# Optimization experiments

Hardware: AMD Instinct MI355X
Metric: run time of the kernel (lower is better)

The kernel has to match this reference:

```python
import jax, jax.numpy as jnp
import numpy as np

TOPK = 300
NUM_LEVELS = 3
GATE_TEMP = 1.0


def _normalized_grid(h, w):
    # matches torch: linspace(-1,1) meshgrid 'ij', stack (xx, yy) -> [h*w, 2]
    y = jnp.linspace(-1.0, 1.0, h, dtype=jnp.float32)
    x = jnp.linspace(-1.0, 1.0, w, dtype=jnp.float32)
    yy, xx = jnp.meshgrid(y, x, indexing='ij')
    return jnp.stack((xx, yy), axis=-1).reshape(h * w, 2)


def setup_inputs() -> dict:
    key = jax.random.key(0)
    ks = jax.random.split(key, 10)
    C, H_DIM, MAXL = 256, 256, 8
    shapes = [(8, C, 100, 152), (8, C, 50, 76), (8, C, 25, 38)]
    inp = {}
    for i, s in enumerate(shapes):
        inp[f'f{i}'] = jax.random.normal(ks[i], s, dtype=jnp.float32)
    inp['conv_w'] = jax.random.normal(ks[3], (C,), dtype=jnp.float32) * (1.0 / np.sqrt(C))
    inp['conv_b'] = jnp.zeros((1,), dtype=jnp.float32)
    inp['level_emb'] = jax.random.normal(ks[4], (MAXL, H_DIM), dtype=jnp.float32)
    qin = C + H_DIM + 3  # 515
    inp['w1'] = jax.random.normal(ks[5], (qin, H_DIM), dtype=jnp.float32) * (1.0 / np.sqrt(qin))
    inp['b1'] = jnp.zeros((H_DIM,), dtype=jnp.float32)
    inp['w2'] = jax.random.normal(ks[6], (H_DIM, H_DIM), dtype=jnp.float32) * (1.0 / np.sqrt(H_DIM))
    inp['b2'] = jnp.zeros((H_DIM,), dtype=jnp.float32)
    inp['gate_w'] = jax.random.normal(ks[7], (H_DIM, MAXL), dtype=jnp.float32) * (1.0 / np.sqrt(H_DIM))
    inp['gate_b'] = jnp.zeros((MAXL,), dtype=jnp.float32)
    inp['residual_scale'] = jnp.zeros((1,), dtype=jnp.float32)  # residual_scale_init=0.0
    return inp


def reference(f0, f1, f2, conv_w, conv_b, level_emb, w1, b1, w2, b2, gate_w, gate_b, residual_scale):
    levels = [f0, f1, f2]
    B = f0.shape[0]
    tok_s, tok_f, tok_p, tok_l = [], [], [], []
    for i, f in enumerate(levels):
        _, C, H, W = f.shape
        # 1x1 conv proxy objectness score -> [B, H*W]
        s = jnp.einsum('bchw,c->bhw', f, conv_w).reshape(B, H * W) + conv_b[0]
        tok_s.append(s)
        tok_f.append(f.reshape(B, C, H * W).transpose(0, 2, 1))       # [B, HW, C]
        tok_p.append(jnp.broadcast_to(_normalized_grid(H, W), (B, H * W, 2)))
        tok_l.append(jnp.full((B, H * W), i, dtype=jnp.int32))
    scores = jnp.concatenate(tok_s, axis=1)   # [B, N]
    feats = jnp.concatenate(tok_f, axis=1)    # [B, N, C]
    pos = jnp.concatenate(tok_p, axis=1)      # [B, N, 2]
    lvl = jnp.concatenate(tok_l, axis=1)      # [B, N]

    top_vals, top_idx = jax.lax.top_k(scores, TOPK)                     # [B, K]
    fk = jnp.take_along_axis(feats, top_idx[:, :, None], axis=1)        # [B, K, C]
    pk = jnp.take_along_axis(pos, top_idx[:, :, None], axis=1)          # [B, K, 2]
    lk = jnp.take_along_axis(lvl, top_idx, axis=1)                      # [B, K]
    sp = jax.nn.sigmoid(top_vals)                                       # [B, K]

    q = jnp.concatenate([fk, level_emb[lk], pk, sp[..., None]], axis=-1)  # [B, K, C+H+3]
    h = jax.nn.relu(q @ w1 + b1)
    h = jax.nn.relu(h @ w2 + b2)
    logits = (h @ gate_w + gate_b)[..., :NUM_LEVELS]                     # [B, K, L]
    gates = jax.nn.softmax(logits / GATE_TEMP, axis=-1)
    alpha = gates.mean(axis=1)                                           # [B, L]
    scale = 1.0 + residual_scale[0] * alpha                              # [B, L]

    outs = [f * scale[:, i][:, None, None, None] for i, f in enumerate(levels)]
    # flatten the output feature dict into one [B, sum(C*H*W)] array
    return jnp.concatenate([o.reshape(B, -1) for o in outs], axis=1)
```

## Files before the change

### kernel.cpp

```cpp
#include <hip/hip_runtime.h>
#include <hip/hip_bf16.h>

#define NTOK 19950
#define KTOP 300
#define NB 8
#define NQ (NB * KTOP)
#define QDIM 520
#define SCW 5225

typedef float f32x4 __attribute__((ext_vector_type(4)));

__device__ __forceinline__ uint32_t fkey(float f) {
    uint32_t u = __float_as_uint(f);
    return (u & 0x80000000u) ? ~u : (u | 0x80000000u);
}

__global__ __launch_bounds__(256) void score_kernel(
    const float* __restrict__ f0, const float* __restrict__ f1, const float* __restrict__ f2,
    const float* __restrict__ conv_w, const float* __restrict__ conv_b,
    float* __restrict__ scores)
{
    __shared__ float cw[256];
    cw[threadIdx.x] = conv_w[threadIdx.x];
    __syncthreads();
    int t = blockIdx.x * 256 + threadIdx.x;
    if (t >= NB * SCW) return;
    const int b = t / SCW;
    const int r = t - b * SCW;
    const float cb = conv_b[0];
    if (r < 3800) {
        const float* base = f0 + (size_t)b * 256 * 15200 + r * 4;
        float s0 = 0.f, s1 = 0.f, s2 = 0.f, s3 = 0.f;
        #pragma unroll 16
        for (int c = 0; c < 256; ++c) {
            float4 v = *reinterpret_cast<const float4*>(base + (size_t)c * 15200);
            float w = cw[c];
            s0 += v.x * w; s1 += v.y * w; s2 += v.z * w; s3 += v.w * w;
        }
        float* so = scores + b * NTOK + r * 4;
        so[0] = s0 + cb; so[1] = s1 + cb; so[2] = s2 + cb; so[3] = s3 + cb;
    } else if (r < 4750) {
        const int r1 = r - 3800;
        const float* base = f1 + (size_t)b * 256 * 3800 + r1 * 4;
        float s0 = 0.f, s1 = 0.f, s2 = 0.f, s3 = 0.f;
        #pragma unroll 16
        for (int c = 0; c < 256; ++c) {
            float4 v = *reinterpret_cast<const float4*>(base + (size_t)c * 3800);
            float w = cw[c];
            s0 += v.x * w; s1 += v.y * w; s2 += v.z * w; s3 += v.w * w;
        }
        float* so = scores + b * NTOK + 15200 + r1 * 4;
        so[0] = s0 + cb; so[1] = s1 + cb; so[2] = s2 + cb; so[3] = s3 + cb;
    } else {
        const int r2 = r - 4750;
        const float* base = f2 + (size_t)b * 256 * 950 + r2 * 2;
        float s0 = 0.f, s1 = 0.f;
        #pragma unroll 16
        for (int c = 0; c < 256; ++c) {
            float2 v = *reinterpret_cast<const float2*>(base + (size_t)c * 950);
            float w = cw[c];
            s0 += v.x * w; s1 += v.y * w;
        }
        float* so = scores + b * NTOK + 19000 + r2 * 2;
        so[0] = s0 + cb; so[1] = s1 + cb;
    }
}

__global__ __launch_bounds__(1024, 1) void topk_kernel(
    const float* __restrict__ scores, int* __restrict__ top_idx)
{
    __shared__ uint32_t key[NTOK];
    __shared__ int whist[16][256];
    __shared__ int suffix[257];
    __shared__ uint32_t s_prefix;
    __shared__ int s_Kr, s_cnt, s_tcnt;
    __shared__ int tie[1024];
    const int tid = threadIdx.x;
    const int wv = tid >> 6;
    const int b = blockIdx.x;
    const float* srow = scores + b * NTOK;
    for (int i = tid; i < NTOK; i += 1024) key[i] = fkey(srow[i]);
    if (tid == 0) { s_prefix = 0u; s_Kr = KTOP; suffix[256] = 0; }
    __syncthreads();
    uint32_t pmask = 0u;
    for (int pass = 0; pass < 4; ++pass) {
        const int shift = 24 - 8 * pass;
        for (int i = tid; i < 16 * 256; i += 1024) ((int*)whist)[i] = 0;
        __syncthreads();
        const uint32_t prefix = s_prefix;
        const int Kr = s_Kr;
        for (int i = tid; i < NTOK; i += 1024) {
            uint32_t k = key[i];
            if ((k & pmask) == prefix) atomicAdd(&whist[wv][(k >> shift) & 255], 1);
        }
        __syncthreads();
        if (tid < 256) {
            int s = 0;
            #pragma unroll
            for (int w = 0; w < 16; ++w) s += whist[w][tid];
            suffix[tid] = s;
        }
        __syncthreads();
        if (tid < 64) {
            const int c0 = suffix[tid * 4], c1 = suffix[tid * 4 + 1];
            const int c2 = suffix[tid * 4 + 2], c3 = suffix[tid * 4 + 3];
            const int tot = c0 + c1 + c2 + c3;
            int s = tot;
            #pragma unroll
            for (int off = 1; off < 64; off <<= 1) {
                int o = __shfl_down(s, off);
                if (tid + off < 64) s += o;
            }
            const int Sn = s - tot;
            suffix[tid * 4 + 3] = c3 + Sn;
            suffix[tid * 4 + 2] = c2 + c3 + Sn;
            suffix[tid * 4 + 1] = c1 + c2 + c3 + Sn;
            suffix[tid * 4 + 0] = tot + Sn;
        }
        __syncthreads();
        if (tid < 256) {
            int sgeq = suffix[tid];
            int sgt  = suffix[tid + 1];
            if (sgeq >= Kr && sgt < Kr) {
                s_prefix = prefix | ((uint32_t)tid << shift);
                s_Kr = Kr - sgt;
            }
        }
        __syncthreads();
        pmask |= (0xFFu << shift);
    }
    const uint32_t T = s_prefix;
    const int need = s_Kr;
    if (tid == 0) { s_cnt = 0; s_tcnt = 0; }
    __syncthreads();
    for (int i = tid; i < NTOK; i += 1024) {
        uint32_t k = key[i];
        if (k > T) {
            int p = atomicAdd(&s_cnt, 1);
            top_idx[b * KTOP + p] = i;
        } else if (k == T) {
            int p = atomicAdd(&s_tcnt, 1);
            if (p < 1024) tie[p] = i;
        }
    }
    __syncthreads();
    if (tid == 0) {
        int base = s_cnt;
        int tcnt = s_tcnt > 1024 ? 1024 : s_tcnt;
        for (int s = 0; s < need; ++s) {
            int mi = s;
            for (int u = s + 1; u < tcnt; ++u) if (tie[u] < tie[mi]) mi = u;
            int tmp = tie[s]; tie[s] = tie[mi]; tie[mi] = tmp;
            top_idx[b * KTOP + base + s] = tie[s];
        }
    }
}

#define QT 8
__global__ __launch_bounds__(512, 1) void mlp_kernel(
    const float* __restrict__ f0, const float* __restrict__ f1, const float* __restrict__ f2,
    const float* __restrict__ scores, const int* __restrict__ top_idx,
    const float* __restrict__ level_emb,
    const float* __restrict__ w1, const float* __restrict__ b1,
    const float* __restrict__ w2, const float* __restrict__ b2,
    const float* __restrict__ gate_w, const float* __restrict__ gate_b,
    float* __restrict__ G)
{
    __shared__ __align__(16) float q[QT][QDIM];
    __shared__ __align__(16) float part[QT][256];
    __shared__ __align__(16) float h[QT][256];
    __shared__ int s_b[QT], s_lvl[QT], s_hw[QT], s_HW[QT];
    const int tid = threadIdx.x;
    const int out = tid & 255;
    const int kh = tid >> 8;
    const int k0 = blockIdx.x * QT;

    if (tid < QT) {
        const int kk = k0 + tid;
        const int bq = kk / KTOP;
        const int idx = top_idx[kk];
        int lvl, hw, HWl, Wl, Hl;
        if (idx < 15200)      { lvl = 0; hw = idx;         HWl = 15200; Wl = 152; Hl = 100; }
        else if (idx < 19000) { lvl = 1; hw = idx - 15200; HWl = 3800;  Wl = 76;  Hl = 50;  }
        else                  { lvl = 2; hw = idx - 19000; HWl = 950;   Wl = 38;  Hl = 25;  }
        s_b[tid] = bq; s_lvl[tid] = lvl; s_hw[tid] = hw; s_HW[tid] = HWl;
        int hh = hw / Wl, ww = hw - hh * Wl;
        float x = -1.0f + 2.0f * (float)ww / (float)(Wl - 1);
        float y = -1.0f + 2.0f * (float)hh / (float)(Hl - 1);
        float sv = scores[bq * NTOK + idx];
        float sp = 1.0f / (1.0f + expf(-sv));
        q[tid][512] = x; q[tid][513] = y; q[tid][514] = sp;
        q[tid][515] = 0.0f; q[tid][516] = 0.0f; q[tid][517] = 0.0f;
        q[tid][518] = 0.0f; q[tid][519] = 0.0f;
    }
    __syncthreads();
    #pragma unroll
    for (int j = tid; j < QT * 256; j += 512) {
        const int t = j >> 8, c = j & 255;
        const int lvl = s_lvl[t];
        const float* f = (lvl == 0) ? f0 : ((lvl == 1) ? f1 : f2);
        q[t][c]       = f[((size_t)(s_b[t] * 256 + c)) * s_HW[t] + s_hw[t]];
        q[t][256 + c] = level_emb[lvl * 256 + c];
    }
    __syncthreads();

    float acc[QT];

    {
        #pragma unroll
        for (int t = 0; t < QT; ++t) acc[t] = 0.0f;
        const float* wp = w1 + (size_t)(kh * 256) * 256 + out;
        float a0 = wp[0], a1 = wp[256], a2 = wp[512], a3 = wp[768];
        for (int i4 = 0; i4 < 64; ++i4) {
            float c0 = a0, c1 = a1, c2 = a2, c3 = a3;
            const float* wn = wp + 1024;
            if (i4 < 63) { a0 = wn[0]; a1 = wn[256]; a2 = wn[512]; a3 = wn[768]; }
            wp = wn;
            const int kb = kh * 256 + i4 * 4;
            #pragma unroll
            for (int t = 0; t < QT; ++t) {
                float4 qv = *reinterpret_cast<const float4*>(&q[t][kb]);
                acc[t] += qv.x * c0 + qv.y * c1 + qv.z * c2 + qv.w * c3;
            }
        }
        if (kh) {
            for (int r = 512; r < 515; ++r) {
                float wv = w1[(size_t)r * 256 + out];
                #pragma unroll
                for (int t = 0; t < QT; ++t) acc[t] += q[t][r] * wv;
            }
            #pragma unroll
            for (int t = 0; t < QT; ++t) part[t][out] = acc[t];
        }
    }
    __syncthreads();
    if (kh == 0) {
        float bj = b1[out];
        #pragma unroll
        for (int t = 0; t < QT; ++t) h[t][out] = fmaxf(acc[t] + part[t][out] + bj, 0.0f);
    }
    __syncthreads();

    {
        #pragma unroll
        for (int t = 0; t < QT; ++t) acc[t] = 0.0f;
        const float* wp = w2 + (size_t)(kh * 128) * 256 + out;
        float a0 = wp[0], a1 = wp[256], a2 = wp[512], a3 = wp[768];
        for (int i4 = 0; i4 < 32; ++i4) {
            float c0 = a0, c1 = a1, c2 = a2, c3 = a3;
            const float* wn = wp + 1024;
            if (i4 < 31) { a0 = wn[0]; a1 = wn[256]; a2 = wn[512]; a3 = wn[768]; }
            wp = wn;
            const int kb = kh * 128 + i4 * 4;
            #pragma unroll
            for (int t = 0; t < QT; ++t) {
                float4 hv = *reinterpret_cast<const float4*>(&h[t][kb]);
                acc[t] += hv.x * c0 + hv.y * c1 + hv.z * c2 + hv.w * c3;
            }
        }
        if (kh) {
            #pragma unroll
            for (int t = 0; t < QT; ++t) part[t][out] = acc[t];
        }
    }
    __syncthreads();
    if (kh == 0) {
        float bj = b2[out];
        #pragma unroll
        for (int t = 0; t < QT; ++t) q[t][out] = fmaxf(acc[t] + part[t][out] + bj, 0.0f);
    }
    __syncthreads();

    if (tid < 256) {
        const int t = tid >> 5, seg = tid & 31;
        float l0 = 0.f, l1 = 0.f, l2 = 0.f;
        for (int c = seg * 8; c < seg * 8 + 8; ++c) {
            float hv = q[t][c];
            l0 += hv * gate_w[c * 8 + 0];
            l1 += hv * gate_w[c * 8 + 1];
            l2 += hv * gate_w[c * 8 + 2];
        }
        float* gp = &part[0][0];
        gp[(t * 32 + seg) * 3 + 0] = l0;
        gp[(t * 32 + seg) * 3 + 1] = l1;
        gp[(t * 32 + seg) * 3 + 2] = l2;
    }
    __syncthreads();
    if (tid < QT) {
        const int t = tid;
        float l0 = gate_b[0], l1 = gate_b[1], l2 = gate_b[2];
        const float* gp = &part[0][0];
        for (int seg = 0; seg < 32; ++seg) {
            l0 += gp[(t * 32 + seg) * 3 + 0];
            l1 += gp[(t * 32 + seg) * 3 + 1];
            l2 += gp[(t * 32 + seg) * 3 + 2];
        }
        float m = fmaxf(l0, fmaxf(l1, l2));
        float e0 = expf(l0 - m), e1 = expf(l1 - m), e2 = expf(l2 - m);
        float inv = 1.0f / (e0 + e1 + e2);
        G[(k0 + t) * 3 + 0] = e0 * inv;
        G[(k0 + t) * 3 + 1] = e1 * inv;
        G[(k0 + t) * 3 + 2] = e2 * inv;
    }
}

__global__ __launch_bounds__(256) void out_kernel(
    const f32x4* __restrict__ f0, const f32x4* __restrict__ f1, const f32x4* __restrict__ f2,
    const float* __restrict__ G, const float* __restrict__ rs, f32x4* __restrict__ out)
{
    __shared__ float red[3][32];
    __shared__ float ssc[3];
    const int b = blockIdx.y;
    const int tid = threadIdx.x;
    if (tid < 96) {
        const int l = tid / 32, c = tid % 32;
        float s = 0.0f;
        const int kb = c * 10;
        const int ke = (kb + 10 < KTOP) ? kb + 10 : KTOP;
        for (int k = kb; k < ke; ++k) s += G[(size_t)(b * KTOP + k) * 3 + l];
        red[l][c] = s;
    }
    __syncthreads();
    for (int off = 16; off > 0; off >>= 1) {
        if (tid < 96) {
            const int l = tid / 32, c = tid % 32;
            if (c < off) red[l][c] += red[l][c + off];
        }
        __syncthreads();
    }
    if (tid < 3) ssc[tid] = 1.0f + rs[0] * (red[tid][0] / (float)KTOP);
    __syncthreads();

    const int t0 = blockIdx.x * 256 + tid;
    const int TPB = gridDim.x * 256;
    f32x4* ob = out + (size_t)b * 1276800;
    {
        const float sc = ssc[0];
        const f32x4* src = f0 + (size_t)b * 972800;
        for (int r = t0; r < 972800; r += TPB)
            __builtin_nontemporal_store(src[r] * sc, &ob[r]);
    }
    {
        const float sc = ssc[1];
        const f32x4* src = f1 + (size_t)b * 243200;
        f32x4* o1 = ob + 972800;
        for (int r = t0; r < 243200; r += TPB)
            __builtin_nontemporal_store(src[r] * sc, &o1[r]);
    }
    {
        const float sc = ssc[2];
        const f32x4* src = f2 + (size_t)b * 60800;
        f32x4* o2 = ob + 1216000;
        for (int r = t0; r < 60800; r += TPB)
            __builtin_nontemporal_store(src[r] * sc, &o2[r]);
    }
}

extern "C" void kernel_launch(void* const* d_in, const int* in_sizes, int n_in,
                              void* d_out, int out_size, void* d_ws, size_t ws_size,
                              hipStream_t stream)
{
    const float* f0        = (const float*)d_in[0];
    const float* f1        = (const float*)d_in[1];
    const float* f2        = (const float*)d_in[2];
    const float* conv_w    = (const float*)d_in[3];
    const float* conv_b    = (const float*)d_in[4];
    const float* level_emb = (const float*)d_in[5];
    const float* w1        = (const float*)d_in[6];
    const float* b1        = (const float*)d_in[7];
    const float* w2        = (const float*)d_in[8];
    const float* b2        = (const float*)d_in[9];
    const float* gate_w    = (const float*)d_in[10];
    const float* gate_b    = (const float*)d_in[11];
    const float* rs        = (const float*)d_in[12];

    char* ws = (char*)d_ws;
    float* scores   = (float*)ws;
    int*   top_idx  = (int*)(ws + 640 * 1024);
    float* G        = (float*)(ws + 656 * 1024);

    score_kernel<<<(NB * SCW + 255) / 256, 256, 0, stream>>>(
        f0, f1, f2, conv_w, conv_b, scores);
    topk_kernel<<<NB, 1024, 0, stream>>>(scores, top_idx);
    mlp_kernel<<<NQ / QT, 512, 0, stream>>>(f0, f1, f2, scores, top_idx, level_emb,
                                            w1, b1, w2, b2, gate_w, gate_b, G);
    out_kernel<<<dim3(256, NB), 256, 0, stream>>>((const f32x4*)f0, (const f32x4*)f1,
                                                  (const f32x4*)f2, G, rs, (f32x4*)d_out);
}
```

Baseline: 161.8 us.

## Split score conv over channel chunks with partial sums and separate reduce

The 1x1 conv score computation now splits the 256 channels into 8 chunks of 32 across 384 blocks. Each block writes partial sums to a workspace buffer, and a new reduce kernel adds the eight partials plus the bias. The goal is more parallelism and shorter per-thread dependency chains than the old one-thread-per-4-pixels loop over all channels. The cost is an extra kernel launch and an extra round trip of partial sums through global memory.

```diff
diff --git a/kernel.cpp b/kernel.cpp
--- a/kernel.cpp
+++ b/kernel.cpp
@@ -2,11 +2,12 @@
 #include <hip/hip_bf16.h>
 
 #define NTOK 19950
+#define NTOKP 19968
 #define KTOP 300
 #define NB 8
-#define NQ (NB * KTOP)
+#define NQ 2400
 #define QDIM 520
-#define SCW 5225
+#define NCC 8
 
 typedef float f32x4 __attribute__((ext_vector_type(4)));
 
@@ -15,55 +16,80 @@
     return (u & 0x80000000u) ? ~u : (u | 0x80000000u);
 }
 
-__global__ __launch_bounds__(256) void score_kernel(
+__global__ __launch_bounds__(256) void score_part_kernel(
     const float* __restrict__ f0, const float* __restrict__ f1, const float* __restrict__ f2,
-    const float* __restrict__ conv_w, const float* __restrict__ conv_b,
+    const float* __restrict__ conv_w, float* __restrict__ partial)
+{
+    __shared__ float cwch[32];
+    const int tid = threadIdx.x;
+    const int blk = blockIdx.x;
+    int b, cc;
+    if (blk < 256)      { b = blk >> 5; cc = (blk >> 2) & 7; }
+    else if (blk < 320) { int i = blk - 256; b = i >> 3; cc = i & 7; }
+    else                { int i = blk - 320; b = i >> 3; cc = i & 7; }
+    if (tid < 32) cwch[tid] = conv_w[cc * 32 + tid];
+    __syncthreads();
+
+    if (blk < 256) {
+        const int q = blk & 3;
+        const f32x4* b4 = (const f32x4*)(f0 + ((size_t)(b * 256 + cc * 32)) * 15200) + q * 950;
+        const int s3 = (tid + 768 < 950) ? tid + 768 : 0;
+        f32x4 a0 = {0,0,0,0}, a1 = a0, a2 = a0, a3 = a0;
+        #pragma unroll 4
+        for (int c = 0; c < 32; ++c) {
+            const f32x4* r = b4 + (size_t)c * 3800;
+            const float w = cwch[c];
+            f32x4 v0 = r[tid], v1 = r[tid + 256], v2 = r[tid + 512], v3 = r[s3];
+            a0 += v0 * w; a1 += v1 * w; a2 += v2 * w; a3 += v3 * w;
+        }
+        f32x4* o4 = (f32x4*)(partial + (size_t)(cc * NB + b) * NTOKP) + q * 950;
+        o4[tid] = a0; o4[tid + 256] = a1; o4[tid + 512] = a2;
+        if (tid + 768 < 950) o4[tid + 768] = a3;
+    } else if (blk < 320) {
+        const f32x4* b4 = (const f32x4*)(f1 + ((size_t)(b * 256 + cc * 32)) * 3800);
+        const int s3 = (tid + 768 < 950) ? tid + 768 : 0;
+        f32x4 a0 = {0,0,0,0}, a1 = a0, a2 = a0, a3 = a0;
+        #pragma unroll 4
+        for (int c = 0; c < 32; ++c) {
+            const f32x4* r = b4 + (size_t)c * 950;
+            const float w = cwch[c];
+            f32x4 v0 = r[tid], v1 = r[tid + 256], v2 = r[tid + 512], v3 = r[s3];
+            a0 += v0 * w; a1 += v1 * w; a2 += v2 * w; a3 += v3 * w;
+        }
+        f32x4* o4 = (f32x4*)(partial + (size_t)(cc * NB + b) * NTOKP + 15200);
+        o4[tid] = a0; o4[tid + 256] = a1; o4[tid + 512] = a2;
+        if (tid + 768 < 950) o4[tid + 768] = a3;
+    } else {
+        const float2* b2 = (const float2*)(f2 + ((size_t)(b * 256 + cc * 32)) * 950);
+        const int s1 = (tid + 256 < 475) ? tid + 256 : 0;
+        float2 a0 = {0,0}, a1 = a0;
+        #pragma unroll 4
+        for (int c = 0; c < 32; ++c) {
+            const float2* r = b2 + (size_t)c * 475;
+            const float w = cwch[c];
+            float2 v0 = r[tid], v1 = r[s1];
+            a0.x += v0.x * w; a0.y += v0.y * w;
+            a1.x += v1.x * w; a1.y += v1.y * w;
+        }
+        float2* o2 = (float2*)(partial + (size_t)(cc * NB + b) * NTOKP + 19000);
+        if (tid < 475) o2[tid] = a0;
+        if (tid + 256 < 475) o2[tid + 256] = a1;
+    }
+}
+
+__global__ __launch_bounds__(256) void score_reduce_kernel(
+    const float* __restrict__ partial, const float* __restrict__ conv_b,
     float* __restrict__ scores)
 {
-    __shared__ float cw[256];
-    cw[threadIdx.x] = conv_w[threadIdx.x];
-    __syncthreads();
-    int t = blockIdx.x * 256 + threadIdx.x;
-    if (t >= NB * SCW) return;
-    const int b = t / SCW;
-    const int r = t - b * SCW;
-    const float cb = conv_b[0];
-    if (r < 3800) {
-        const float* base = f0 + (size_t)b * 256 * 15200 + r * 4;
-        float s0 = 0.f, s1 = 0.f, s2 = 0.f, s3 = 0.f;
-        #pragma unroll 16
-        for (int c = 0; c < 256; ++c) {
-            float4 v = *reinterpret_cast<const float4*>(base + (size_t)c * 15200);
-            float w = cw[c];
-            s0 += v.x * w; s1 += v.y * w; s2 += v.z * w; s3 += v.w * w;
-        }
-        float* so = scores + b * NTOK + r * 4;
-        so[0] = s0 + cb; so[1] = s1 + cb; so[2] = s2 + cb; so[3] = s3 + cb;
-    } else if (r < 4750) {
-        const int r1 = r - 3800;
-        const float* base = f1 + (size_t)b * 256 * 3800 + r1 * 4;
-        float s0 = 0.f, s1 = 0.f, s2 = 0.f, s3 = 0.f;
-        #pragma unroll 16
-        for (int c = 0; c < 256; ++c) {
-            float4 v = *reinterpret_cast<const float4*>(base + (size_t)c * 3800);
-            float w = cw[c];
-            s0 += v.x * w; s1 += v.y * w; s2 += v.z * w; s3 += v.w * w;
-        }
-        float* so = scores + b * NTOK + 15200 + r1 * 4;
-        so[0] = s0 + cb; so[1] = s1 + cb; so[2] = s2 + cb; so[3] = s3 + cb;
-    } else {
-        const int r2 = r - 4750;
-        const float* base = f2 + (size_t)b * 256 * 950 + r2 * 2;
-        float s0 = 0.f, s1 = 0.f;
-        #pragma unroll 16
-        for (int c = 0; c < 256; ++c) {
-            float2 v = *reinterpret_cast<const float2*>(base + (size_t)c * 950);
-            float w = cw[c];
-            s0 += v.x * w; s1 += v.y * w;
-        }
-        float* so = scores + b * NTOK + 19000 + r2 * 2;
-        so[0] = s0 + cb; so[1] = s1 + cb;
-    }
+    const int t = blockIdx.x * 256 + threadIdx.x;
+    if (t >= NB * NTOK) return;
+    const int b = t / NTOK;
+    const int i = t - b * NTOK;
+    float s = 0.0f;
+    #pragma unroll
+    for (int cc = 0; cc < NCC; ++cc)
+        s += partial[(size_t)(cc * NB + b) * NTOKP + i];
+    scores[t] = s + conv_b[0];
 }
 
 __global__ __launch_bounds__(1024, 1) void topk_kernel(
@@ -375,12 +401,13 @@
     const float* rs        = (const float*)d_in[12];
 
     char* ws = (char*)d_ws;
-    float* scores   = (float*)ws;
-    int*   top_idx  = (int*)(ws + 640 * 1024);
-    float* G        = (float*)(ws + 656 * 1024);
-
-    score_kernel<<<(NB * SCW + 255) / 256, 256, 0, stream>>>(
-        f0, f1, f2, conv_w, conv_b, scores);
+    float* scores  = (float*)ws;
+    int*   top_idx = (int*)(ws + 640 * 1024);
+    float* G       = (float*)(ws + 656 * 1024);
+    float* partial = (float*)(ws + 704 * 1024);
+
+    score_part_kernel<<<384, 256, 0, stream>>>(f0, f1, f2, conv_w, partial);
+    score_reduce_kernel<<<(NB * NTOK + 255) / 256, 256, 0, stream>>>(partial, conv_b, scores);
     topk_kernel<<<NB, 1024, 0, stream>>>(scores, top_idx);
     mlp_kernel<<<NQ / QT, 512, 0, stream>>>(f0, f1, f2, scores, top_idx, level_emb,
                                             w1, b1, w2, b2, gate_w, gate_b, G);
```

After: 156.8 us. 1.03x faster.
